# Kernel optimization log

Hardware: AMD Instinct MI355X
Metric: run time of the kernel (lower is better)

## Reference

```python
import jax, jax.numpy as jnp
import numpy as np

B, F, D = 1024, 16, 64
P = F * (F - 1) // 2  # 120 field pairs


def setup_inputs() -> dict:
    key = jax.random.key(0)
    k1, k2, k3 = jax.random.split(key, 3)
    x = jax.random.normal(k1, (B, F, D), dtype=jnp.float32)
    # torch Linear weight layout: [out_features, in_features] = [D, D*D], one per pair
    W = jax.random.normal(k2, (P, D, D * D), dtype=jnp.float32) * (1.0 / np.sqrt(D * D))
    b = jax.random.normal(k3, (P, D), dtype=jnp.float32) * 0.01
    return {"x": x, "W": W, "b": b}


def reference(x, W, b):
    # x: [B, F, D]; W: [P, D, D*D]; b: [P, D]
    Bs, Fs, Ds = x.shape
    Ps = W.shape[0]
    ii, jj = np.triu_indices(Fs, k=1)  # pair order matches nested (i, j>i) loop
    xi = x[:, ii, :]  # [B, P, D] -> left vector of outer product
    xj = x[:, jj, :]  # [B, P, D] -> right vector
    # Flattened outer tmp[b, a*D + c] = xi[b,p,a] * xj[b,p,c];
    # Linear: out = tmp @ W^T + b. Reshape W to [P, D_out, a, c] and fuse,
    # never materializing the [B, P, D*D] outer-product tensor.
    W3 = W.reshape(Ps, Ds, Ds, Ds)
    out = jnp.einsum('bpa,bpc,pkac->bpk', xi, xj, W3) + b[None, :, :]
    return out  # [B, P, D]
```

## Files before the change

kernel.cpp:

```cpp
#include <hip/hip_runtime.h>
#include <stdint.h>
#include <stddef.h>

constexpr int NB = 1024;
constexpr int NF = 16;
constexpr int ND = 64;
constexpr int NP = 120;
constexpr int KD = ND * ND;
constexpr int OUT_STRIDE = NP * ND;

using floatx4  = __attribute__((ext_vector_type(4))) float;
using short8   = __attribute__((ext_vector_type(8))) short;
using uint4v   = __attribute__((ext_vector_type(4))) uint32_t;
using ushort4v = __attribute__((ext_vector_type(4))) uint16_t;

constexpr int XT_STRIDE = 264;
constexpr int BT_STRIDE = 72;
constexpr int BT_BUF    = ND * BT_STRIDE;

__device__ __forceinline__ uint32_t pack_bf16(float f0, float f1) {
    uint32_t u0 = __float_as_uint(f0) + 0x8000u;
    uint32_t u1 = __float_as_uint(f1) + 0x8000u;
    return __builtin_amdgcn_perm(u1, u0, 0x07060302u);
}
__device__ __forceinline__ uint16_t to_bf16(float f) {
    return (uint16_t)((__float_as_uint(f) + 0x8000u) >> 16);
}
__device__ __forceinline__ float from_bf16(uint16_t u) {
    return __uint_as_float(((uint32_t)u) << 16);
}

__global__ __launch_bounds__(256, 2)
void outer_kernel(const float* __restrict__ x, const float* __restrict__ W,
                  const float* __restrict__ bias, float* __restrict__ out)
{
    __shared__ uint16_t lds_xit[ND * XT_STRIDE];
    __shared__ uint16_t lds_bt[2 * BT_BUF];

    const int p  = blockIdx.x;
    const int b0 = blockIdx.y * 256;

    int icol = 0, rem = p;
    while (rem >= NF - 1 - icol) { rem -= NF - 1 - icol; ++icol; }
    const int jcol = icol + 1 + rem;

    const int t    = threadIdx.x;
    const int wave = t >> 6;
    const int lane = t & 63;
    const int r    = lane & 15;
    const int quad = lane >> 4;

    {
        const float* src = x + (size_t)(b0 + t) * (NF * ND) + icol * ND;
        #pragma unroll
        for (int c = 0; c < ND; c += 4) {
            floatx4 v = *(const floatx4*)(src + c);
            lds_xit[(c + 0) * XT_STRIDE + t] = to_bf16(v.x);
            lds_xit[(c + 1) * XT_STRIDE + t] = to_bf16(v.y);
            lds_xit[(c + 2) * XT_STRIDE + t] = to_bf16(v.z);
            lds_xit[(c + 3) * XT_STRIDE + t] = to_bf16(v.w);
        }
    }

    short8 afrag[4][2];
    #pragma unroll
    for (int ms = 0; ms < 4; ++ms) {
        const float* srow = x + (size_t)(b0 + wave*64 + ms*16 + r) * (NF * ND)
                              + jcol * ND + quad * 8;
        #pragma unroll
        for (int ks = 0; ks < 2; ++ks) {
            floatx4 v0 = *(const floatx4*)(srow + ks * 32);
            floatx4 v1 = *(const floatx4*)(srow + ks * 32 + 4);
            union { short8 s; uint32_t u[4]; } af;
            af.u[0] = pack_bf16(v0.x, v0.y);
            af.u[1] = pack_bf16(v0.z, v0.w);
            af.u[2] = pack_bf16(v1.x, v1.y);
            af.u[3] = pack_bf16(v1.z, v1.w);
            afrag[ms][ks] = af.s;
        }
    }

    const int n_st = t >> 2;
    const int c_st = (t & 3) * 16;
    const float* wsrc = W + ((size_t)p * ND + n_st) * KD + c_st;
    uint16_t* bdst0 = &lds_bt[n_st * BT_STRIDE + c_st];

    floatx4 wreg[4];

    #pragma unroll
    for (int q = 0; q < 4; ++q) wreg[q] = *(const floatx4*)(wsrc + q * 4);
    {
        uint4v q0 = (uint4v){ pack_bf16(wreg[0].x, wreg[0].y), pack_bf16(wreg[0].z, wreg[0].w),
                              pack_bf16(wreg[1].x, wreg[1].y), pack_bf16(wreg[1].z, wreg[1].w) };
        uint4v q1 = (uint4v){ pack_bf16(wreg[2].x, wreg[2].y), pack_bf16(wreg[2].z, wreg[2].w),
                              pack_bf16(wreg[3].x, wreg[3].y), pack_bf16(wreg[3].z, wreg[3].w) };
        *(uint4v*)(bdst0)     = q0;
        *(uint4v*)(bdst0 + 8) = q1;
    }
    #pragma unroll
    for (int q = 0; q < 4; ++q) wreg[q] = *(const floatx4*)(wsrc + ND + q * 4);
    __syncthreads();

    floatx4 acc[4][4] = {};
    const floatx4 zerof = (floatx4){0.f, 0.f, 0.f, 0.f};

    #pragma unroll 1
    for (int a = 0; a < ND; ++a) {
        const int cur = a & 1;
        const uint16_t* rbuf = lds_bt + cur * BT_BUF;

        float xiv[4][4];
        #pragma unroll
        for (int ms = 0; ms < 4; ++ms) {
            ushort4v xu = *(const ushort4v*)&lds_xit[a * XT_STRIDE
                                                     + wave*64 + ms*16 + quad*4];
            xiv[ms][0] = from_bf16(xu.x);
            xiv[ms][1] = from_bf16(xu.y);
            xiv[ms][2] = from_bf16(xu.z);
            xiv[ms][3] = from_bf16(xu.w);
        }

        #pragma unroll
        for (int ns = 0; ns < 4; ++ns) {
            const int brow = (ns*16 + r) * BT_STRIDE + quad * 8;
            short8 bf0 = *(const short8*)&rbuf[brow];
            short8 bf1 = *(const short8*)&rbuf[brow + 32];
            #pragma unroll
            for (int ms = 0; ms < 4; ++ms) {
                floatx4 tv = __builtin_amdgcn_mfma_f32_16x16x32_bf16(
                    afrag[ms][0], bf0, zerof, 0, 0, 0);
                tv = __builtin_amdgcn_mfma_f32_16x16x32_bf16(
                    afrag[ms][1], bf1, tv, 0, 0, 0);
                #pragma unroll
                for (int reg = 0; reg < 4; ++reg)
                    acc[ms][ns][reg] = __builtin_fmaf(xiv[ms][reg], tv[reg],
                                                      acc[ms][ns][reg]);
            }
        }

        if (a + 1 < ND) {
            uint16_t* bd = bdst0 + (cur ^ 1) * BT_BUF;
            uint4v q0 = (uint4v){ pack_bf16(wreg[0].x, wreg[0].y), pack_bf16(wreg[0].z, wreg[0].w),
                                  pack_bf16(wreg[1].x, wreg[1].y), pack_bf16(wreg[1].z, wreg[1].w) };
            uint4v q1 = (uint4v){ pack_bf16(wreg[2].x, wreg[2].y), pack_bf16(wreg[2].z, wreg[2].w),
                                  pack_bf16(wreg[3].x, wreg[3].y), pack_bf16(wreg[3].z, wreg[3].w) };
            *(uint4v*)(bd)     = q0;
            *(uint4v*)(bd + 8) = q1;
        }
        if (a + 2 < ND) {
            const float* wn = wsrc + (size_t)(a + 2) * ND;
            #pragma unroll
            for (int q = 0; q < 4; ++q) wreg[q] = *(const floatx4*)(wn + q * 4);
        }

        __syncthreads();
    }

    #pragma unroll
    for (int ns = 0; ns < 4; ++ns) {
        const float bb = bias[p * ND + ns*16 + r];
        #pragma unroll
        for (int ms = 0; ms < 4; ++ms) {
            #pragma unroll
            for (int reg = 0; reg < 4; ++reg) {
                const int row = b0 + wave*64 + ms*16 + quad*4 + reg;
                out[(size_t)row * OUT_STRIDE + p * ND + ns*16 + r]
                    = acc[ms][ns][reg] + bb;
            }
        }
    }
}

extern "C" void kernel_launch(void* const* d_in, const int* in_sizes, int n_in,
                              void* d_out, int out_size, void* d_ws, size_t ws_size,
                              hipStream_t stream) {
    const float* x    = (const float*)d_in[0];
    const float* W    = (const float*)d_in[1];
    const float* bias = (const float*)d_in[2];
    float* out = (float*)d_out;

    dim3 grid(NP, NB / 256);
    outer_kernel<<<grid, 256, 0, stream>>>(x, W, bias, out);
}
```

Before: 224.0 us.

## Process two reduction steps per barrier with deeper W prefetch

Restructures the main loop so each iteration stages two rows of W into LDS and runs two compute steps between barriers, halving the number of __syncthreads calls. Global loads of W are issued two rows ahead, and the LDS store for the next pair is moved before the compute. This adds register pressure (eight float4 prefetch registers) and doubles the LDS weight buffer, which may affect occupancy under the 2-blocks-per-CU launch bound.

```diff
diff --git a/kernel.cpp b/kernel.cpp
--- a/kernel.cpp
+++ b/kernel.cpp
@@ -30,12 +30,21 @@
     return __uint_as_float(((uint32_t)u) << 16);
 }
 
+__device__ __forceinline__ void pack_store(uint16_t* bd, const floatx4* wr) {
+    uint4v q0 = (uint4v){ pack_bf16(wr[0].x, wr[0].y), pack_bf16(wr[0].z, wr[0].w),
+                          pack_bf16(wr[1].x, wr[1].y), pack_bf16(wr[1].z, wr[1].w) };
+    uint4v q1 = (uint4v){ pack_bf16(wr[2].x, wr[2].y), pack_bf16(wr[2].z, wr[2].w),
+                          pack_bf16(wr[3].x, wr[3].y), pack_bf16(wr[3].z, wr[3].w) };
+    *(uint4v*)(bd)     = q0;
+    *(uint4v*)(bd + 8) = q1;
+}
+
 __global__ __launch_bounds__(256, 2)
 void outer_kernel(const float* __restrict__ x, const float* __restrict__ W,
                   const float* __restrict__ bias, float* __restrict__ out)
 {
     __shared__ uint16_t lds_xit[ND * XT_STRIDE];
-    __shared__ uint16_t lds_bt[2 * BT_BUF];
+    __shared__ uint16_t lds_bt[2][2][BT_BUF];
 
     const int p  = blockIdx.x;
     const int b0 = blockIdx.y * 256;
@@ -83,32 +92,26 @@
     const int n_st = t >> 2;
     const int c_st = (t & 3) * 16;
     const float* wsrc = W + ((size_t)p * ND + n_st) * KD + c_st;
-    uint16_t* bdst0 = &lds_bt[n_st * BT_STRIDE + c_st];
+    const int woff = n_st * BT_STRIDE + c_st;
 
-    floatx4 wreg[4];
+    floatx4 wreg[8];
 
     #pragma unroll
     for (int q = 0; q < 4; ++q) wreg[q] = *(const floatx4*)(wsrc + q * 4);
-    {
-        uint4v q0 = (uint4v){ pack_bf16(wreg[0].x, wreg[0].y), pack_bf16(wreg[0].z, wreg[0].w),
-                              pack_bf16(wreg[1].x, wreg[1].y), pack_bf16(wreg[1].z, wreg[1].w) };
-        uint4v q1 = (uint4v){ pack_bf16(wreg[2].x, wreg[2].y), pack_bf16(wreg[2].z, wreg[2].w),
-                              pack_bf16(wreg[3].x, wreg[3].y), pack_bf16(wreg[3].z, wreg[3].w) };
-        *(uint4v*)(bdst0)     = q0;
-        *(uint4v*)(bdst0 + 8) = q1;
-    }
+    pack_store(&lds_bt[0][0][woff], &wreg[0]);
     #pragma unroll
     for (int q = 0; q < 4; ++q) wreg[q] = *(const floatx4*)(wsrc + ND + q * 4);
+    pack_store(&lds_bt[0][1][woff], &wreg[0]);
+    #pragma unroll
+    for (int q = 0; q < 4; ++q) wreg[q]     = *(const floatx4*)(wsrc + 2 * ND + q * 4);
+    #pragma unroll
+    for (int q = 0; q < 4; ++q) wreg[4 + q] = *(const floatx4*)(wsrc + 3 * ND + q * 4);
     __syncthreads();
 
     floatx4 acc[4][4] = {};
     const floatx4 zerof = (floatx4){0.f, 0.f, 0.f, 0.f};
 
-    #pragma unroll 1
-    for (int a = 0; a < ND; ++a) {
-        const int cur = a & 1;
-        const uint16_t* rbuf = lds_bt + cur * BT_BUF;
-
+    auto compute_step = [&](int a, const uint16_t* rbuf) {
         float xiv[4][4];
         #pragma unroll
         for (int ms = 0; ms < 4; ++ms) {
@@ -119,7 +122,6 @@
             xiv[ms][2] = from_bf16(xu.z);
             xiv[ms][3] = from_bf16(xu.w);
         }
-
         #pragma unroll
         for (int ns = 0; ns < 4; ++ns) {
             const int brow = (ns*16 + r) * BT_STRIDE + quad * 8;
@@ -137,22 +139,25 @@
                                                       acc[ms][ns][reg]);
             }
         }
+    };
 
-        if (a + 1 < ND) {
-            uint16_t* bd = bdst0 + (cur ^ 1) * BT_BUF;
-            uint4v q0 = (uint4v){ pack_bf16(wreg[0].x, wreg[0].y), pack_bf16(wreg[0].z, wreg[0].w),
-                                  pack_bf16(wreg[1].x, wreg[1].y), pack_bf16(wreg[1].z, wreg[1].w) };
-            uint4v q1 = (uint4v){ pack_bf16(wreg[2].x, wreg[2].y), pack_bf16(wreg[2].z, wreg[2].w),
-                                  pack_bf16(wreg[3].x, wreg[3].y), pack_bf16(wreg[3].z, wreg[3].w) };
-            *(uint4v*)(bd)     = q0;
-            *(uint4v*)(bd + 8) = q1;
+    #pragma unroll 1
+    for (int t2 = 0; t2 < ND / 2; ++t2) {
+        const int cur = t2 & 1;
+
+        if (t2 < ND/2 - 1) {
+            pack_store(&lds_bt[cur ^ 1][0][woff], &wreg[0]);
+            pack_store(&lds_bt[cur ^ 1][1][woff], &wreg[4]);
         }
-        if (a + 2 < ND) {
-            const float* wn = wsrc + (size_t)(a + 2) * ND;
+        if (t2 < ND/2 - 2) {
+            const float* wn = wsrc + (size_t)(2*t2 + 4) * ND;
             #pragma unroll
-            for (int q = 0; q < 4; ++q) wreg[q] = *(const floatx4*)(wn + q * 4);
+            for (int q = 0; q < 4; ++q) wreg[q]     = *(const floatx4*)(wn + q * 4);
+            #pragma unroll
+            for (int q = 0; q < 4; ++q) wreg[4 + q] = *(const floatx4*)(wn + ND + q * 4);
         }
-
+        compute_step(2*t2,     &lds_bt[cur][0][0]);
+        compute_step(2*t2 + 1, &lds_bt[cur][1][0]);
         __syncthreads();
     }
 
```

Measured after the change: 264.6 us. +18.1%, slower.

## Store W tiles in LDS in MFMA fragment order and use lighter barrier

Applied to the files above, without the earlier changes.

Rewrites the per-step W tile staging so each thread writes its 16-element chunk directly in the lane order the MFMA B-fragment reads need. Every lane then reads its fragment at a contiguous lane*8 offset, with no padded row stride and fewer bank conflicts. The xi unpack becomes vectorized shift/mask operations, and the accumulate becomes a vector FMA. __syncthreads is replaced by a manual LDS-only waitcnt plus s_barrier, so the outstanding global W prefetch is not waited on at each step. The risk is the hand-coded waitcnt encoding and synchronization correctness.

```diff
diff --git a/kernel.cpp b/kernel.cpp
--- a/kernel.cpp
+++ b/kernel.cpp
@@ -12,11 +12,10 @@
 using floatx4  = __attribute__((ext_vector_type(4))) float;
 using short8   = __attribute__((ext_vector_type(8))) short;
 using uint4v   = __attribute__((ext_vector_type(4))) uint32_t;
-using ushort4v = __attribute__((ext_vector_type(4))) uint16_t;
+using uint2v   = __attribute__((ext_vector_type(2))) uint32_t;
 
 constexpr int XT_STRIDE = 264;
-constexpr int BT_STRIDE = 72;
-constexpr int BT_BUF    = ND * BT_STRIDE;
+constexpr int BT_HALF   = 4096;
 
 __device__ __forceinline__ uint32_t pack_bf16(float f0, float f1) {
     uint32_t u0 = __float_as_uint(f0) + 0x8000u;
@@ -26,16 +25,19 @@
 __device__ __forceinline__ uint16_t to_bf16(float f) {
     return (uint16_t)((__float_as_uint(f) + 0x8000u) >> 16);
 }
-__device__ __forceinline__ float from_bf16(uint16_t u) {
-    return __uint_as_float(((uint32_t)u) << 16);
+
+__device__ __forceinline__ void pack_store16(uint16_t* bd, floatx4 a, floatx4 b) {
+    uint4v q = (uint4v){ pack_bf16(a.x, a.y), pack_bf16(a.z, a.w),
+                         pack_bf16(b.x, b.y), pack_bf16(b.z, b.w) };
+    *(uint4v*)(bd) = q;
 }
 
 __global__ __launch_bounds__(256, 2)
 void outer_kernel(const float* __restrict__ x, const float* __restrict__ W,
                   const float* __restrict__ bias, float* __restrict__ out)
 {
-    __shared__ uint16_t lds_xit[ND * XT_STRIDE];
-    __shared__ uint16_t lds_bt[2 * BT_BUF];
+    __shared__ __align__(16) uint16_t lds_xit[ND * XT_STRIDE];
+    __shared__ __align__(16) uint16_t lds_bt[2 * BT_HALF];
 
     const int p  = blockIdx.x;
     const int b0 = blockIdx.y * 256;
@@ -80,80 +82,84 @@
         }
     }
 
-    const int n_st = t >> 2;
-    const int c_st = (t & 3) * 16;
-    const float* wsrc = W + ((size_t)p * ND + n_st) * KD + c_st;
-    uint16_t* bdst0 = &lds_bt[n_st * BT_STRIDE + c_st];
+    const int ks_w   = (t >> 6) & 1;
+    const int quad_w = (t >> 4) & 3;
+    const int r_w    = t & 15;
+    const int c0_w   = ks_w * 32 + quad_w * 8;
+    const int n0_w   = ((t >> 7) + 0) * 16 + r_w;
+    const int n1_w   = ((t >> 7) + 2) * 16 + r_w;
+    const float* wp0 = W + ((size_t)p * ND + n0_w) * KD + c0_w;
+    const float* wp1 = W + ((size_t)p * ND + n1_w) * KD + c0_w;
+    uint16_t* wst0 = &lds_bt[(size_t)t * 8];
+    uint16_t* wst1 = &lds_bt[(size_t)(256 + t) * 8];
 
     floatx4 wreg[4];
 
-    #pragma unroll
-    for (int q = 0; q < 4; ++q) wreg[q] = *(const floatx4*)(wsrc + q * 4);
-    {
-        uint4v q0 = (uint4v){ pack_bf16(wreg[0].x, wreg[0].y), pack_bf16(wreg[0].z, wreg[0].w),
-                              pack_bf16(wreg[1].x, wreg[1].y), pack_bf16(wreg[1].z, wreg[1].w) };
-        uint4v q1 = (uint4v){ pack_bf16(wreg[2].x, wreg[2].y), pack_bf16(wreg[2].z, wreg[2].w),
-                              pack_bf16(wreg[3].x, wreg[3].y), pack_bf16(wreg[3].z, wreg[3].w) };
-        *(uint4v*)(bdst0)     = q0;
-        *(uint4v*)(bdst0 + 8) = q1;
-    }
-    #pragma unroll
-    for (int q = 0; q < 4; ++q) wreg[q] = *(const floatx4*)(wsrc + ND + q * 4);
+    wreg[0] = *(const floatx4*)(wp0);
+    wreg[1] = *(const floatx4*)(wp0 + 4);
+    wreg[2] = *(const floatx4*)(wp1);
+    wreg[3] = *(const floatx4*)(wp1 + 4);
+    pack_store16(wst0, wreg[0], wreg[1]);
+    pack_store16(wst1, wreg[2], wreg[3]);
+    wreg[0] = *(const floatx4*)(wp0 + ND);
+    wreg[1] = *(const floatx4*)(wp0 + ND + 4);
+    wreg[2] = *(const floatx4*)(wp1 + ND);
+    wreg[3] = *(const floatx4*)(wp1 + ND + 4);
     __syncthreads();
 
     floatx4 acc[4][4] = {};
     const floatx4 zerof = (floatx4){0.f, 0.f, 0.f, 0.f};
+    const uint16_t* rb_lane = lds_bt + (size_t)lane * 8;
 
     #pragma unroll 1
     for (int a = 0; a < ND; ++a) {
         const int cur = a & 1;
-        const uint16_t* rbuf = lds_bt + cur * BT_BUF;
+        const uint16_t* rbuf = rb_lane + cur * BT_HALF;
 
-        float xiv[4][4];
+        floatx4 xiv[4];
         #pragma unroll
         for (int ms = 0; ms < 4; ++ms) {
-            ushort4v xu = *(const ushort4v*)&lds_xit[a * XT_STRIDE
-                                                     + wave*64 + ms*16 + quad*4];
-            xiv[ms][0] = from_bf16(xu.x);
-            xiv[ms][1] = from_bf16(xu.y);
-            xiv[ms][2] = from_bf16(xu.z);
-            xiv[ms][3] = from_bf16(xu.w);
+            uint2v xu = *(const uint2v*)&lds_xit[a * XT_STRIDE
+                                                 + wave*64 + ms*16 + quad*4];
+            xiv[ms] = (floatx4){ __uint_as_float(xu.x << 16),
+                                 __uint_as_float(xu.x & 0xffff0000u),
+                                 __uint_as_float(xu.y << 16),
+                                 __uint_as_float(xu.y & 0xffff0000u) };
         }
 
         #pragma unroll
         for (int ns = 0; ns < 4; ++ns) {
-            const int brow = (ns*16 + r) * BT_STRIDE + quad * 8;
-            short8 bf0 = *(const short8*)&rbuf[brow];
-            short8 bf1 = *(const short8*)&rbuf[brow + 32];
+            short8 bf0 = *(const short8*)(rbuf + (ns*2 + 0) * 512);
+            short8 bf1 = *(const short8*)(rbuf + (ns*2 + 1) * 512);
             #pragma unroll
             for (int ms = 0; ms < 4; ++ms) {
                 floatx4 tv = __builtin_amdgcn_mfma_f32_16x16x32_bf16(
                     afrag[ms][0], bf0, zerof, 0, 0, 0);
                 tv = __builtin_amdgcn_mfma_f32_16x16x32_bf16(
                     afrag[ms][1], bf1, tv, 0, 0, 0);
-                #pragma unroll
-                for (int reg = 0; reg < 4; ++reg)
-                    acc[ms][ns][reg] = __builtin_fmaf(xiv[ms][reg], tv[reg],
-                                                      acc[ms][ns][reg]);
+                acc[ms][ns] += xiv[ms] * tv;
             }
         }
 
         if (a + 1 < ND) {
-            uint16_t* bd = bdst0 + (cur ^ 1) * BT_BUF;
-            uint4v q0 = (uint4v){ pack_bf16(wreg[0].x, wreg[0].y), pack_bf16(wreg[0].z, wreg[0].w),
-                                  pack_bf16(wreg[1].x, wreg[1].y), pack_bf16(wreg[1].z, wreg[1].w) };
-            uint4v q1 = (uint4v){ pack_bf16(wreg[2].x, wreg[2].y), pack_bf16(wreg[2].z, wreg[2].w),
-                                  pack_bf16(wreg[3].x, wreg[3].y), pack_bf16(wreg[3].z, wreg[3].w) };
-            *(uint4v*)(bd)     = q0;
-            *(uint4v*)(bd + 8) = q1;
+            uint16_t* bd0 = wst0 + (cur ^ 1) * BT_HALF;
+            uint16_t* bd1 = wst1 + (cur ^ 1) * BT_HALF;
+            pack_store16(bd0, wreg[0], wreg[1]);
+            pack_store16(bd1, wreg[2], wreg[3]);
         }
         if (a + 2 < ND) {
-            const float* wn = wsrc + (size_t)(a + 2) * ND;
-            #pragma unroll
-            for (int q = 0; q < 4; ++q) wreg[q] = *(const floatx4*)(wn + q * 4);
+            const float* s0 = wp0 + (size_t)(a + 2) * ND;
+            const float* s1 = wp1 + (size_t)(a + 2) * ND;
+            wreg[0] = *(const floatx4*)(s0);
+            wreg[1] = *(const floatx4*)(s0 + 4);
+            wreg[2] = *(const floatx4*)(s1);
+            wreg[3] = *(const floatx4*)(s1 + 4);
         }
 
-        __syncthreads();
+        asm volatile("" ::: "memory");
+        __builtin_amdgcn_s_waitcnt(0xC07F);
+        __builtin_amdgcn_s_barrier();
+        asm volatile("" ::: "memory");
     }
 
     #pragma unroll
```

Result: no change. 226.0 us (+0.9%).
